# Optimization experiments

Measured on AMD Instinct MI355X. Metric: run time of the kernel, lower is better.

The kernel has to match this reference:

```python
import jax, jax.numpy as jnp
import numpy as np

N, E, D_IN, D_HID, D_OUT = 50000, 800000, 128, 128, 64

def setup_inputs() -> dict:
    key = jax.random.key(0)
    ks = jax.random.split(key, 20)
    inp = {
        'x': jax.random.normal(ks[0], (N, D_IN), dtype=jnp.float32),
        'edge_index': jax.random.randint(ks[1], (2, E), 0, N, dtype=jnp.int64),
        'edge_attr': jax.random.normal(ks[2], (E, 16), dtype=jnp.float32),
        'edge_weight': jax.random.uniform(ks[3], (E,), dtype=jnp.float32),
    }
    dims = [(D_IN, D_HID), (D_HID, D_HID), (D_HID, D_OUT)]
    for i, (di, do) in enumerate(dims):
        s = 1.0 / np.sqrt(di)
        inp[f'Wl{i}'] = jax.random.uniform(ks[4 + 5 * i], (di, do), minval=-s, maxval=s, dtype=jnp.float32)
        inp[f'bl{i}'] = jnp.zeros((do,), dtype=jnp.float32)
        inp[f'Wr{i}'] = jax.random.uniform(ks[5 + 5 * i], (di, do), minval=-s, maxval=s, dtype=jnp.float32)
        inp[f'Ws{i}'] = jax.random.uniform(ks[6 + 5 * i], (di, do), minval=-s, maxval=s, dtype=jnp.float32)
        inp[f'bs{i}'] = jnp.zeros((do,), dtype=jnp.float32)
    return inp


def _sage(x, src, dst, Wl, bl, Wr):
    # mean aggregation of source features at target nodes (PyG SAGEConv)
    msg = x[src]                                               # [E, d] gather
    ssum = jax.ops.segment_sum(msg, dst, num_segments=N)        # [N, d]
    cnt = jax.ops.segment_sum(jnp.ones((src.shape[0],), x.dtype), dst, num_segments=N)
    agg = ssum / jnp.maximum(cnt, 1.0)[:, None]
    return agg @ Wl + bl + x @ Wr                               # lin_l(agg) + lin_r(x)


def reference(x, edge_index, edge_attr, edge_weight,
              Wl0, bl0, Wr0, Ws0, bs0,
              Wl1, bl1, Wr1, Ws1, bs1,
              Wl2, bl2, Wr2, Ws2, bs2):
    src, dst = edge_index[0], edge_index[1]
    h = jax.nn.relu(_sage(x, src, dst, Wl0, bl0, Wr0) + x @ Ws0 + bs0)
    h = jax.nn.relu(_sage(h, src, dst, Wl1, bl1, Wr1) + h @ Ws1 + bs1)
    out = _sage(h, src, dst, Wl2, bl2, Wr2) + h @ Ws2 + bs2
    return out
```

## Files before the change

### kernel.cpp

```cpp
#include <hip/hip_runtime.h>
#include <hip/hip_bf16.h>


#define LB __launch_bounds__

typedef __attribute__((ext_vector_type(8))) short short8;
typedef __attribute__((ext_vector_type(4))) float f32x4;

__device__ __forceinline__ unsigned short bf16_rne(float f) {
  unsigned u = __builtin_bit_cast(unsigned, f);
  unsigned r = u + 0x7fffu + ((u >> 16) & 1u);
  return (unsigned short)(r >> 16);
}
__device__ __forceinline__ float bf16_to_f(unsigned short us) {
  return __builtin_bit_cast(float, (unsigned)us << 16);
}
__device__ __forceinline__ float bits_to_f(unsigned u) {
  return __builtin_bit_cast(float, u);
}

#define BCAP 8192
#define P1_CHUNK 4096

__global__ LB(256) void p1_bucket(const int* __restrict__ src, const int* __restrict__ dst,
                                  int* __restrict__ bcnt, int2* __restrict__ pairs, int E) {
  __shared__ int cnt[256];
  __shared__ int base[256];
  const int tid = threadIdx.x;
  cnt[tid] = 0;
  __syncthreads();
  const int e0 = blockIdx.x * P1_CHUNK;
  int myb[16], myr[16], mys[16], myd[16];
#pragma unroll
  for (int i = 0; i < 16; ++i) {
    int e = e0 + i * 256 + tid;
    myb[i] = -1;
    if (e < E) {
      int s = src[e], d = dst[e];
      int b = d >> 8;
      myb[i] = b;
      mys[i] = s;
      myd[i] = d;
      myr[i] = atomicAdd(&cnt[b], 1);
    }
  }
  __syncthreads();
  base[tid] = (cnt[tid] > 0) ? atomicAdd(&bcnt[tid], cnt[tid]) : 0;
  __syncthreads();
#pragma unroll
  for (int i = 0; i < 16; ++i) {
    int b = myb[i];
    if (b >= 0) {
      int p = base[b] + myr[i];
      if (p < BCAP) pairs[(size_t)b * BCAP + p] = make_int2(mys[i], myd[i]);
    }
  }
}

__global__ LB(256) void p2_hist_scan(const int2* __restrict__ pairs, const int* __restrict__ bcnt,
                                     int* __restrict__ row_ptr, float* __restrict__ scale,
                                     int* __restrict__ btot, int N) {
  __shared__ int h[256];
  __shared__ int sc[256];
  const int tid = threadIdx.x;
  const int b = blockIdx.x;
  h[tid] = 0;
  __syncthreads();
  int m = bcnt[b];
  if (m > BCAP) m = BCAP;
  for (int i = tid; i < m; i += 256) {
    int d = pairs[(size_t)b * BCAP + i].y;
    atomicAdd(&h[d & 255], 1);
  }
  __syncthreads();
  int deg = h[tid];
  sc[tid] = deg;
  __syncthreads();
  for (int off = 1; off < 256; off <<= 1) {
    int add = (tid >= off) ? sc[tid - off] : 0;
    __syncthreads();
    sc[tid] += add;
    __syncthreads();
  }
  int node = b * 256 + tid;
  if (node < N) {
    row_ptr[node] = sc[tid] - deg;
    scale[node] = 1.0f / (float)(deg > 1 ? deg : 1);
  }
  if (tid == 255) btot[b] = sc[255];
}

__global__ LB(256) void scan_b(const int* __restrict__ btot, int* __restrict__ bbase,
                               int* __restrict__ row_ptr_N, int NB) {
  __shared__ int sc[256];
  const int t = threadIdx.x;
  int v = (t < NB) ? btot[t] : 0;
  sc[t] = v;
  __syncthreads();
  for (int off = 1; off < 256; off <<= 1) {
    int add = (t >= off) ? sc[t - off] : 0;
    __syncthreads();
    sc[t] += add;
    __syncthreads();
  }
  if (t < NB) bbase[t] = sc[t] - v;
  if (t == 255) *row_ptr_N = sc[255];
}

__global__ LB(256) void p4_place(const int2* __restrict__ pairs, const int* __restrict__ bcnt,
                                 const int* __restrict__ bbase, int* __restrict__ row_ptr,
                                 int* __restrict__ srcs, int N) {
  __shared__ int cur[256];
  const int tid = threadIdx.x;
  const int b = blockIdx.x;
  const int node = b * 256 + tid;
  const int bb = bbase[b];
  if (node < N) {
    int abs_off = bb + row_ptr[node];
    row_ptr[node] = abs_off;
    cur[tid] = abs_off;
  } else {
    cur[tid] = 0;
  }
  __syncthreads();
  int m = bcnt[b];
  if (m > BCAP) m = BCAP;
  for (int i = tid; i < m; i += 256) {
    int2 pr = pairs[(size_t)b * BCAP + i];
    int p = atomicAdd(&cur[pr.y & 255], 1);
    srcs[p] = pr.x;
  }
}

__global__ LB(256) void wpack_all(const float* __restrict__ Wl0, const float* __restrict__ Wr0,
                                  const float* __restrict__ Ws0, const float* __restrict__ bl0,
                                  const float* __restrict__ bs0, const float* __restrict__ Wl1,
                                  const float* __restrict__ Wr1, const float* __restrict__ Ws1,
                                  const float* __restrict__ bl1, const float* __restrict__ bs1,
                                  const float* __restrict__ Wl2, const float* __restrict__ Wr2,
                                  const float* __restrict__ Ws2, const float* __restrict__ bl2,
                                  const float* __restrict__ bs2, ushort* __restrict__ Bh0,
                                  ushort* __restrict__ Bo0, float* __restrict__ bb0,
                                  ushort* __restrict__ Bh1, ushort* __restrict__ Bo1,
                                  float* __restrict__ bb1, ushort* __restrict__ Bh2,
                                  ushort* __restrict__ Bo2, float* __restrict__ bb2) {
  const int layer = blockIdx.y;
  const float *Wl, *Wr, *Ws, *bl, *bs;
  ushort *Bh, *Bo;
  float* bb;
  int M;
  if (layer == 0) {
    Wl = Wl0; Wr = Wr0; Ws = Ws0; bl = bl0; bs = bs0; Bh = Bh0; Bo = Bo0; bb = bb0; M = 256;
  } else if (layer == 1) {
    Wl = Wl1; Wr = Wr1; Ws = Ws1; bl = bl1; bs = bs1; Bh = Bh1; Bo = Bo1; bb = bb1; M = 256;
  } else {
    Wl = Wl2; Wr = Wr2; Ws = Ws2; bl = bl2; bs = bs2; Bh = Bh2; Bo = Bo2; bb = bb2; M = 128;
  }
  const int DO = M / 2;
  int idx = blockIdx.x * 256 + threadIdx.x;
  if (idx < 128 * M) {
    int k = idx / M, c = idx - k * M;
    float v = (c < DO) ? Wl[k * DO + c] : (Wr[k * DO + (c - DO)] + Ws[k * DO + (c - DO)]);
    unsigned short h = bf16_rne(v);
    unsigned short l = bf16_rne(v - bf16_to_f(h));
    int d = ((k >> 3) * M + c) * 8 + (k & 7);
    Bh[d] = h;
    Bo[d] = l;
  }
  if (idx < DO) bb[idx] = bl[idx] + bs[idx];
}

__device__ __forceinline__ void split8(const float* __restrict__ p, short8& h, short8& l) {
  float4 f0 = *(const float4*)p;
  float4 f1 = *(const float4*)(p + 4);
  float f[8] = {f0.x, f0.y, f0.z, f0.w, f1.x, f1.y, f1.z, f1.w};
#pragma unroll
  for (int j = 0; j < 8; ++j) {
    unsigned u = __builtin_bit_cast(unsigned, f[j]);
    h[j] = (short)(u >> 16);
    l[j] = (short)bf16_rne(f[j] - bits_to_f(u & 0xffff0000u));
  }
}

template <int M, bool AFP32>
__global__ LB(256, 2) void mfma_gemm_kernel(const float* __restrict__ Af,
                                            const ushort* __restrict__ Ahi,
                                            const ushort* __restrict__ Alo,
                                            const ushort* __restrict__ Bhi,
                                            const ushort* __restrict__ Blo,
                                            ushort* __restrict__ Yb, float* __restrict__ Z, int n) {
  constexpr int DO = M / 2;
  constexpr int NWC = M / 64;
  constexpr int NWR = 4 / NWC;
  const int tid = threadIdx.x;
  const int w = tid >> 6, l = tid & 63;
  const int q = l >> 4, m16 = l & 15;
  const int rowBase = blockIdx.x * (64 * NWR) + (w / NWC) * 64;
  const int colBase = (w % NWC) * 64;

  f32x4 acc[4][4] = {};
  int rrow[4];
#pragma unroll
  for (int i = 0; i < 4; ++i) {
    int r = rowBase + i * 16 + m16;
    rrow[i] = r < n ? r : n - 1;
  }

#pragma unroll
  for (int s = 0; s < 4; ++s) {
    const int ka = s * 32 + q * 8;
    short8 ah[4], al[4], bh[4], bo[4];
#pragma unroll
    for (int i = 0; i < 4; ++i) {
      size_t off = (size_t)rrow[i] * 128 + ka;
      if (AFP32) {
        split8(Af + off, ah[i], al[i]);
      } else {
        ah[i] = *(const short8*)(Ahi + off);
        al[i] = *(const short8*)(Alo + off);
      }
    }
    const int kb = s * 4 + q;
#pragma unroll
    for (int j = 0; j < 4; ++j) {
      size_t off = ((size_t)kb * M + colBase + j * 16 + m16) * 8;
      bh[j] = *(const short8*)(Bhi + off);
      bo[j] = *(const short8*)(Blo + off);
    }
#pragma unroll
    for (int i = 0; i < 4; ++i)
#pragma unroll
      for (int j = 0; j < 4; ++j) {
        acc[i][j] = __builtin_amdgcn_mfma_f32_16x16x32_bf16(ah[i], bh[j], acc[i][j], 0, 0, 0);
        acc[i][j] = __builtin_amdgcn_mfma_f32_16x16x32_bf16(ah[i], bo[j], acc[i][j], 0, 0, 0);
        acc[i][j] = __builtin_amdgcn_mfma_f32_16x16x32_bf16(al[i], bh[j], acc[i][j], 0, 0, 0);
      }
  }

#pragma unroll
  for (int i = 0; i < 4; ++i) {
    int rb = rowBase + i * 16 + q * 4;
#pragma unroll
    for (int j = 0; j < 4; ++j) {
      int c = colBase + j * 16 + m16;
#pragma unroll
      for (int r = 0; r < 4; ++r) {
        int row = rb + r;
        if (row < n) {
          float v = acc[i][j][r];
          if (c < DO)
            Yb[(size_t)row * DO + c] = bf16_rne(v);
          else
            Z[(size_t)row * DO + (c - DO)] = v;
        }
      }
    }
  }
}

__global__ LB(256) void agg128_kernel(const ushort* __restrict__ Y, const float* __restrict__ Z,
                                      const int* __restrict__ row_ptr, const int* __restrict__ srcs,
                                      const float* __restrict__ scale,
                                      const float* __restrict__ bsum, unsigned* __restrict__ Hhi,
                                      unsigned* __restrict__ Hlo, int n) {
  int node = blockIdx.x * 4 + (threadIdx.x >> 6);
  if (node >= n) return;
  const int lane = threadIdx.x & 63;
  const int li = lane & 31;
  const int half = lane >> 5;
  const int e0 = row_ptr[node], end = row_ptr[node + 1];
  const int cnt = end - e0;
  const int c1 = cnt < 64 ? cnt : 64;
  int idx = (lane < c1) ? srcs[e0 + lane] : 0;
  const uint2* Yu = (const uint2*)Y;
  float a0 = 0.f, a1 = 0.f, a2 = 0.f, a3 = 0.f;

  int j = 0;
  for (; j + 8 <= c1; j += 8) {
    int s0 = __shfl(idx, j + half);
    int s1 = __shfl(idx, j + 2 + half);
    int s2 = __shfl(idx, j + 4 + half);
    int s3 = __shfl(idx, j + 6 + half);
    uint2 u0 = Yu[(size_t)s0 * 32 + li];
    uint2 u1 = Yu[(size_t)s1 * 32 + li];
    uint2 u2 = Yu[(size_t)s2 * 32 + li];
    uint2 u3 = Yu[(size_t)s3 * 32 + li];
    a0 += bits_to_f(u0.x << 16) + bits_to_f(u1.x << 16) + bits_to_f(u2.x << 16) +
          bits_to_f(u3.x << 16);
    a1 += bits_to_f(u0.x & 0xffff0000u) + bits_to_f(u1.x & 0xffff0000u) +
          bits_to_f(u2.x & 0xffff0000u) + bits_to_f(u3.x & 0xffff0000u);
    a2 += bits_to_f(u0.y << 16) + bits_to_f(u1.y << 16) + bits_to_f(u2.y << 16) +
          bits_to_f(u3.y << 16);
    a3 += bits_to_f(u0.y & 0xffff0000u) + bits_to_f(u1.y & 0xffff0000u) +
          bits_to_f(u2.y & 0xffff0000u) + bits_to_f(u3.y & 0xffff0000u);
  }
  for (; j + 2 <= c1; j += 2) {
    int s = __shfl(idx, j + half);
    uint2 u = Yu[(size_t)s * 32 + li];
    a0 += bits_to_f(u.x << 16);
    a1 += bits_to_f(u.x & 0xffff0000u);
    a2 += bits_to_f(u.y << 16);
    a3 += bits_to_f(u.y & 0xffff0000u);
  }
  if (j < c1) {
    int s = __shfl(idx, j);
    if (half == 0) {
      uint2 u = Yu[(size_t)s * 32 + li];
      a0 += bits_to_f(u.x << 16);
      a1 += bits_to_f(u.x & 0xffff0000u);
      a2 += bits_to_f(u.y << 16);
      a3 += bits_to_f(u.y & 0xffff0000u);
    }
  }
  if (cnt > 64) {
    int e = e0 + 64;
    for (; e + 2 <= end; e += 2) {
      int s = srcs[e + half];
      uint2 u = Yu[(size_t)s * 32 + li];
      a0 += bits_to_f(u.x << 16);
      a1 += bits_to_f(u.x & 0xffff0000u);
      a2 += bits_to_f(u.y << 16);
      a3 += bits_to_f(u.y & 0xffff0000u);
    }
    if (e < end && half == 0) {
      int s = srcs[e];
      uint2 u = Yu[(size_t)s * 32 + li];
      a0 += bits_to_f(u.x << 16);
      a1 += bits_to_f(u.x & 0xffff0000u);
      a2 += bits_to_f(u.y << 16);
      a3 += bits_to_f(u.y & 0xffff0000u);
    }
  }
  a0 += __shfl(a0, lane ^ 32);
  a1 += __shfl(a1, lane ^ 32);
  a2 += __shfl(a2, lane ^ 32);
  a3 += __shfl(a3, lane ^ 32);

  float sc = scale[node];
  float4 z = ((const float4*)Z)[(size_t)node * 32 + li];
  float4 b = ((const float4*)bsum)[li];
  float o0 = fmaxf(z.x + sc * a0 + b.x, 0.f);
  float o1 = fmaxf(z.y + sc * a1 + b.y, 0.f);
  float o2 = fmaxf(z.z + sc * a2 + b.z, 0.f);
  float o3 = fmaxf(z.w + sc * a3 + b.w, 0.f);
  unsigned short h0 = bf16_rne(o0), h1 = bf16_rne(o1), h2 = bf16_rne(o2), h3 = bf16_rne(o3);
  if (half == 0) {
    uint2 hp;
    hp.x = (unsigned)h0 | ((unsigned)h1 << 16);
    hp.y = (unsigned)h2 | ((unsigned)h3 << 16);
    ((uint2*)Hhi)[(size_t)node * 32 + li] = hp;
  } else {
    unsigned short l0 = bf16_rne(o0 - bf16_to_f(h0));
    unsigned short l1 = bf16_rne(o1 - bf16_to_f(h1));
    unsigned short l2 = bf16_rne(o2 - bf16_to_f(h2));
    unsigned short l3 = bf16_rne(o3 - bf16_to_f(h3));
    uint2 lp;
    lp.x = (unsigned)l0 | ((unsigned)l1 << 16);
    lp.y = (unsigned)l2 | ((unsigned)l3 << 16);
    ((uint2*)Hlo)[(size_t)node * 32 + li] = lp;
  }
}

__global__ LB(256) void agg64_kernel(const ushort* __restrict__ Y, const float* __restrict__ Z,
                                     const int* __restrict__ row_ptr, const int* __restrict__ srcs,
                                     const float* __restrict__ scale, const float* __restrict__ bsum,
                                     float* __restrict__ out, int n) {
  int node = blockIdx.x * 4 + (threadIdx.x >> 6);
  if (node >= n) return;
  const int lane = threadIdx.x & 63;
  const int li = lane & 15;
  const int qt = lane >> 4;
  const int e0 = row_ptr[node], end = row_ptr[node + 1];
  const int cnt = end - e0;
  const int c1 = cnt < 64 ? cnt : 64;
  int idx = (lane < c1) ? srcs[e0 + lane] : 0;
  const uint2* Yu = (const uint2*)Y;
  float a0 = 0.f, a1 = 0.f, a2 = 0.f, a3 = 0.f;

  int j = 0;
  for (; j + 16 <= c1; j += 16) {
    int s0 = __shfl(idx, j + qt);
    int s1 = __shfl(idx, j + 4 + qt);
    int s2 = __shfl(idx, j + 8 + qt);
    int s3 = __shfl(idx, j + 12 + qt);
    uint2 u0 = Yu[(size_t)s0 * 16 + li];
    uint2 u1 = Yu[(size_t)s1 * 16 + li];
    uint2 u2 = Yu[(size_t)s2 * 16 + li];
    uint2 u3 = Yu[(size_t)s3 * 16 + li];
    a0 += bits_to_f(u0.x << 16) + bits_to_f(u1.x << 16) + bits_to_f(u2.x << 16) +
          bits_to_f(u3.x << 16);
    a1 += bits_to_f(u0.x & 0xffff0000u) + bits_to_f(u1.x & 0xffff0000u) +
          bits_to_f(u2.x & 0xffff0000u) + bits_to_f(u3.x & 0xffff0000u);
    a2 += bits_to_f(u0.y << 16) + bits_to_f(u1.y << 16) + bits_to_f(u2.y << 16) +
          bits_to_f(u3.y << 16);
    a3 += bits_to_f(u0.y & 0xffff0000u) + bits_to_f(u1.y & 0xffff0000u) +
          bits_to_f(u2.y & 0xffff0000u) + bits_to_f(u3.y & 0xffff0000u);
  }
  for (; j + 4 <= c1; j += 4) {
    int s = __shfl(idx, j + qt);
    uint2 u = Yu[(size_t)s * 16 + li];
    a0 += bits_to_f(u.x << 16);
    a1 += bits_to_f(u.x & 0xffff0000u);
    a2 += bits_to_f(u.y << 16);
    a3 += bits_to_f(u.y & 0xffff0000u);
  }
  {
    int rem = c1 - j;
    if (rem > 0) {
      int s = __shfl(idx, j + (qt < rem ? qt : 0));
      if (qt < rem) {
        uint2 u = Yu[(size_t)s * 16 + li];
        a0 += bits_to_f(u.x << 16);
        a1 += bits_to_f(u.x & 0xffff0000u);
        a2 += bits_to_f(u.y << 16);
        a3 += bits_to_f(u.y & 0xffff0000u);
      }
    }
  }
  if (cnt > 64) {
    int e = e0 + 64;
    for (; e + 4 <= end; e += 4) {
      int s = srcs[e + qt];
      uint2 u = Yu[(size_t)s * 16 + li];
      a0 += bits_to_f(u.x << 16);
      a1 += bits_to_f(u.x & 0xffff0000u);
      a2 += bits_to_f(u.y << 16);
      a3 += bits_to_f(u.y & 0xffff0000u);
    }
    int rem = end - e;
    if (qt < rem) {
      int s = srcs[e + qt];
      uint2 u = Yu[(size_t)s * 16 + li];
      a0 += bits_to_f(u.x << 16);
      a1 += bits_to_f(u.x & 0xffff0000u);
      a2 += bits_to_f(u.y << 16);
      a3 += bits_to_f(u.y & 0xffff0000u);
    }
  }
  a0 += __shfl(a0, lane ^ 16);
  a1 += __shfl(a1, lane ^ 16);
  a2 += __shfl(a2, lane ^ 16);
  a3 += __shfl(a3, lane ^ 16);
  a0 += __shfl(a0, lane ^ 32);
  a1 += __shfl(a1, lane ^ 32);
  a2 += __shfl(a2, lane ^ 32);
  a3 += __shfl(a3, lane ^ 32);

  if (qt == 0) {
    float sc = scale[node];
    float4 z = ((const float4*)Z)[(size_t)node * 16 + li];
    float4 b = ((const float4*)bsum)[li];
    float4 o;
    o.x = z.x + sc * a0 + b.x;
    o.y = z.y + sc * a1 + b.y;
    o.z = z.z + sc * a2 + b.z;
    o.w = z.w + sc * a3 + b.w;
    ((float4*)out)[(size_t)node * 16 + li] = o;
  }
}

extern "C" void kernel_launch(void* const* d_in, const int* in_sizes, int n_in,
                              void* d_out, int out_size, void* d_ws, size_t ws_size,
                              hipStream_t stream) {
  const float* x = (const float*)d_in[0];
  const int* ei = (const int*)d_in[1];
  const int N = in_sizes[0] / 128;
  const int E = in_sizes[3];
  const int* src = ei;
  const int* dst = ei + E;
  const float* Wl[3] = {(const float*)d_in[4], (const float*)d_in[9], (const float*)d_in[14]};
  const float* bl[3] = {(const float*)d_in[5], (const float*)d_in[10], (const float*)d_in[15]};
  const float* Wr[3] = {(const float*)d_in[6], (const float*)d_in[11], (const float*)d_in[16]};
  const float* Ws[3] = {(const float*)d_in[7], (const float*)d_in[12], (const float*)d_in[17]};
  const float* bs[3] = {(const float*)d_in[8], (const float*)d_in[13], (const float*)d_in[18]};

  const int NB = (N + 255) >> 8;

  size_t off = 0;
  auto carve = [&](size_t bytes) -> char* {
    char* p = (char*)d_ws + off;
    off += (bytes + 255) & ~(size_t)255;
    return p;
  };
  int* row_ptr = (int*)carve((size_t)(N + 1) * 4);
  int* bcnt = (int*)carve((size_t)NB * 4);
  int* btot = (int*)carve((size_t)NB * 4);
  int* bbase = (int*)carve((size_t)NB * 4);
  float* scale = (float*)carve((size_t)N * 4);
  int* srcs = (int*)carve((size_t)E * 4);
  int2* pairs = (int2*)carve((size_t)NB * BCAP * 8);
  ushort* Hhi = (ushort*)carve((size_t)N * 128 * 2);
  ushort* Hlo = (ushort*)carve((size_t)N * 128 * 2);
  ushort* Yb = (ushort*)carve((size_t)N * 128 * 2);
  float* Zf = (float*)carve((size_t)N * 128 * 4);
  ushort* Bh[3];
  ushort* Bo[3];
  float* bsum[3];
  for (int i = 0; i < 3; ++i) {
    Bh[i] = (ushort*)carve(128 * 256 * 2);
    Bo[i] = (ushort*)carve(128 * 256 * 2);
    bsum[i] = (float*)carve(128 * 4);
  }
  (void)ws_size;
  (void)n_in;
  (void)out_size;

  hipMemsetAsync(bcnt, 0, (size_t)NB * 4, stream);
  p1_bucket<<<(E + P1_CHUNK - 1) / P1_CHUNK, 256, 0, stream>>>(src, dst, bcnt, pairs, E);
  p2_hist_scan<<<NB, 256, 0, stream>>>(pairs, bcnt, row_ptr, scale, btot, N);
  scan_b<<<1, 256, 0, stream>>>(btot, bbase, row_ptr + N, NB);
  p4_place<<<NB, 256, 0, stream>>>(pairs, bcnt, bbase, row_ptr, srcs, N);

  wpack_all<<<dim3(128, 3), 256, 0, stream>>>(Wl[0], Wr[0], Ws[0], bl[0], bs[0], Wl[1], Wr[1],
                                              Ws[1], bl[1], bs[1], Wl[2], Wr[2], Ws[2], bl[2],
                                              bs[2], Bh[0], Bo[0], bsum[0], Bh[1], Bo[1], bsum[1],
                                              Bh[2], Bo[2], bsum[2]);

  int g64 = (N + 63) / 64;
  int g128 = (N + 127) / 128;
  int gAgg = (N + 3) / 4;

  mfma_gemm_kernel<256, true><<<g64, 256, 0, stream>>>(x, nullptr, nullptr, Bh[0], Bo[0], Yb, Zf, N);
  agg128_kernel<<<gAgg, 256, 0, stream>>>(Yb, Zf, row_ptr, srcs, scale, bsum[0], (unsigned*)Hhi,
                                          (unsigned*)Hlo, N);
  mfma_gemm_kernel<256, false><<<g64, 256, 0, stream>>>(nullptr, Hhi, Hlo, Bh[1], Bo[1], Yb, Zf, N);
  agg128_kernel<<<gAgg, 256, 0, stream>>>(Yb, Zf, row_ptr, srcs, scale, bsum[1], (unsigned*)Hhi,
                                          (unsigned*)Hlo, N);
  mfma_gemm_kernel<128, false><<<g128, 256, 0, stream>>>(nullptr, Hhi, Hlo, Bh[2], Bo[2], Yb, Zf, N);
  agg64_kernel<<<gAgg, 256, 0, stream>>>(Yb, Zf, row_ptr, srcs, scale, bsum[2], (float*)d_out, N);
}
```

Baseline: 337.5 us.

## Fuse CSR histogram, scan and placement into one decoupled-lookback kernel

Merges the per-bucket histogram, the cross-bucket scan and the edge placement kernels into a single kernel. The cross-bucket prefix is computed with a decoupled look-back over per-block status flags. The memset of the bucket counters moves into the weight-packing kernel, which also zeroes the status flags. This removes three kernel launches and the memset. In exchange, correctness relies on spin-waiting across blocks, which assumes earlier blocks get scheduled, though with only 196 blocks this is safe.

Measured after the change: 376.1 us. 1.11x slower.

```diff
diff --git a/kernel.cpp b/kernel.cpp
--- a/kernel.cpp
+++ b/kernel.cpp
@@ -21,6 +21,9 @@
 
 #define BCAP 8192
 #define P1_CHUNK 4096
+#define FLAG_INC 0x80000000u
+#define FLAG_AGG 0x40000000u
+#define VAL_MASK 0x3FFFFFFFu
 
 __global__ LB(256) void p1_bucket(const int* __restrict__ src, const int* __restrict__ dst,
                                   int* __restrict__ bcnt, int2* __restrict__ pairs, int E) {
@@ -57,11 +60,14 @@
   }
 }
 
-__global__ LB(256) void p2_hist_scan(const int2* __restrict__ pairs, const int* __restrict__ bcnt,
-                                     int* __restrict__ row_ptr, float* __restrict__ scale,
-                                     int* __restrict__ btot, int N) {
+__global__ LB(256) void p234_kernel(const int2* __restrict__ pairs, const int* __restrict__ bcnt,
+                                    unsigned* __restrict__ status, int* __restrict__ row_ptr,
+                                    float* __restrict__ scale, int* __restrict__ srcs, int N,
+                                    int NB) {
   __shared__ int h[256];
   __shared__ int sc[256];
+  __shared__ int cur[256];
+  __shared__ int shared_bb;
   const int tid = threadIdx.x;
   const int b = blockIdx.x;
   h[tid] = 0;
@@ -69,11 +75,10 @@
   int m = bcnt[b];
   if (m > BCAP) m = BCAP;
   for (int i = tid; i < m; i += 256) {
-    int d = pairs[(size_t)b * BCAP + i].y;
-    atomicAdd(&h[d & 255], 1);
-  }
-  __syncthreads();
-  int deg = h[tid];
+    atomicAdd(&h[pairs[(size_t)b * BCAP + i].y & 255], 1);
+  }
+  __syncthreads();
+  const int deg = h[tid];
   sc[tid] = deg;
   __syncthreads();
   for (int off = 1; off < 256; off <<= 1) {
@@ -82,49 +87,38 @@
     sc[tid] += add;
     __syncthreads();
   }
-  int node = b * 256 + tid;
+  const int total = sc[255];
+  if (tid == 0) {
+    __hip_atomic_store(&status[b], FLAG_AGG | (unsigned)total, __ATOMIC_RELEASE,
+                       __HIP_MEMORY_SCOPE_AGENT);
+    unsigned ex = 0;
+    for (int j = b - 1; j >= 0;) {
+      unsigned s;
+      do {
+        s = __hip_atomic_load(&status[j], __ATOMIC_ACQUIRE, __HIP_MEMORY_SCOPE_AGENT);
+      } while (s == 0u);
+      if (s & FLAG_INC) {
+        ex += s & VAL_MASK;
+        break;
+      }
+      ex += s & VAL_MASK;
+      --j;
+    }
+    __hip_atomic_store(&status[b], FLAG_INC | ((unsigned)total + ex), __ATOMIC_RELEASE,
+                       __HIP_MEMORY_SCOPE_AGENT);
+    shared_bb = (int)ex;
+    if (b == NB - 1) row_ptr[N] = (int)(ex + (unsigned)total);
+  }
+  __syncthreads();
+  const int bb = shared_bb;
+  const int abs_off = bb + sc[tid] - deg;
+  const int node = b * 256 + tid;
   if (node < N) {
-    row_ptr[node] = sc[tid] - deg;
+    row_ptr[node] = abs_off;
     scale[node] = 1.0f / (float)(deg > 1 ? deg : 1);
   }
-  if (tid == 255) btot[b] = sc[255];
-}
-
-__global__ LB(256) void scan_b(const int* __restrict__ btot, int* __restrict__ bbase,
-                               int* __restrict__ row_ptr_N, int NB) {
-  __shared__ int sc[256];
-  const int t = threadIdx.x;
-  int v = (t < NB) ? btot[t] : 0;
-  sc[t] = v;
-  __syncthreads();
-  for (int off = 1; off < 256; off <<= 1) {
-    int add = (t >= off) ? sc[t - off] : 0;
-    __syncthreads();
-    sc[t] += add;
-    __syncthreads();
-  }
-  if (t < NB) bbase[t] = sc[t] - v;
-  if (t == 255) *row_ptr_N = sc[255];
-}
-
-__global__ LB(256) void p4_place(const int2* __restrict__ pairs, const int* __restrict__ bcnt,
-                                 const int* __restrict__ bbase, int* __restrict__ row_ptr,
-                                 int* __restrict__ srcs, int N) {
-  __shared__ int cur[256];
-  const int tid = threadIdx.x;
-  const int b = blockIdx.x;
-  const int node = b * 256 + tid;
-  const int bb = bbase[b];
-  if (node < N) {
-    int abs_off = bb + row_ptr[node];
-    row_ptr[node] = abs_off;
-    cur[tid] = abs_off;
-  } else {
-    cur[tid] = 0;
-  }
-  __syncthreads();
-  int m = bcnt[b];
-  if (m > BCAP) m = BCAP;
+  cur[tid] = abs_off;
+  __syncthreads();
   for (int i = tid; i < m; i += 256) {
     int2 pr = pairs[(size_t)b * BCAP + i];
     int p = atomicAdd(&cur[pr.y & 255], 1);
@@ -143,8 +137,15 @@
                                   ushort* __restrict__ Bo0, float* __restrict__ bb0,
                                   ushort* __restrict__ Bh1, ushort* __restrict__ Bo1,
                                   float* __restrict__ bb1, ushort* __restrict__ Bh2,
-                                  ushort* __restrict__ Bo2, float* __restrict__ bb2) {
+                                  ushort* __restrict__ Bo2, float* __restrict__ bb2,
+                                  int* __restrict__ bcnt, unsigned* __restrict__ status, int NB) {
   const int layer = blockIdx.y;
+  if (layer == 0 && blockIdx.x == 0) {
+    for (int i = threadIdx.x; i < NB; i += 256) {
+      bcnt[i] = 0;
+      status[i] = 0u;
+    }
+  }
   const float *Wl, *Wr, *Ws, *bl, *bs;
   ushort *Bh, *Bo;
   float* bb;
@@ -484,8 +485,7 @@
   };
   int* row_ptr = (int*)carve((size_t)(N + 1) * 4);
   int* bcnt = (int*)carve((size_t)NB * 4);
-  int* btot = (int*)carve((size_t)NB * 4);
-  int* bbase = (int*)carve((size_t)NB * 4);
+  unsigned* status = (unsigned*)carve((size_t)NB * 4);
   float* scale = (float*)carve((size_t)N * 4);
   int* srcs = (int*)carve((size_t)E * 4);
   int2* pairs = (int2*)carve((size_t)NB * BCAP * 8);
@@ -505,16 +505,12 @@
   (void)n_in;
   (void)out_size;
 
-  hipMemsetAsync(bcnt, 0, (size_t)NB * 4, stream);
-  p1_bucket<<<(E + P1_CHUNK - 1) / P1_CHUNK, 256, 0, stream>>>(src, dst, bcnt, pairs, E);
-  p2_hist_scan<<<NB, 256, 0, stream>>>(pairs, bcnt, row_ptr, scale, btot, N);
-  scan_b<<<1, 256, 0, stream>>>(btot, bbase, row_ptr + N, NB);
-  p4_place<<<NB, 256, 0, stream>>>(pairs, bcnt, bbase, row_ptr, srcs, N);
-
   wpack_all<<<dim3(128, 3), 256, 0, stream>>>(Wl[0], Wr[0], Ws[0], bl[0], bs[0], Wl[1], Wr[1],
                                               Ws[1], bl[1], bs[1], Wl[2], Wr[2], Ws[2], bl[2],
                                               bs[2], Bh[0], Bo[0], bsum[0], Bh[1], Bo[1], bsum[1],
-                                              Bh[2], Bo[2], bsum[2]);
+                                              Bh[2], Bo[2], bsum[2], bcnt, status, NB);
+  p1_bucket<<<(E + P1_CHUNK - 1) / P1_CHUNK, 256, 0, stream>>>(src, dst, bcnt, pairs, E);
+  p234_kernel<<<NB, 256, 0, stream>>>(pairs, bcnt, status, row_ptr, scale, srcs, N, NB);
 
   int g64 = (N + 63) / 64;
   int g128 = (N + 127) / 128;
```
